# Kernel tuning notes

Measured on AMD Instinct MI355X. Metric: run time of the kernel, lower is better.

The kernel has to match this reference:

```python
import jax, jax.numpy as jnp
import numpy as np
from jax import lax

B, T, EPROJS, DUNITS, ATT_DIM = 32, 2048, 1024, 1024, 512
ACONV_CHANS, ACONV_FILTS = 10, 100
KSIZE = 2 * ACONV_FILTS + 1  # 201
SCALING = 2.0


def setup_inputs() -> dict:
    key = jax.random.key(0)
    ks = jax.random.split(key, 16)
    lengths = jax.random.randint(ks[1], (B,), T // 2, T + 1, dtype=jnp.int32)
    # normalized uniform initial attention over valid frames (as in module's init branch)
    mask = jnp.arange(T)[None, :] < lengths[:, None]
    att_prev = mask.astype(jnp.float32) / lengths[:, None].astype(jnp.float32)
    s_e = 1.0 / np.sqrt(EPROJS)
    s_d = 1.0 / np.sqrt(DUNITS)
    s_a = 1.0 / np.sqrt(ATT_DIM)
    s_c = 1.0 / np.sqrt(ACONV_CHANS)
    return {
        "enc_hs_pad": jax.random.normal(ks[0], (B, T, EPROJS), jnp.float32),
        "enc_hs_len": lengths,
        "dec_z": jax.random.normal(ks[2], (B, DUNITS), jnp.float32),
        "att_prev": att_prev,
        "att_h": jax.random.normal(ks[3], (B, ATT_DIM), jnp.float32) * 0.1,
        "att_c": jax.random.normal(ks[4], (B, ATT_DIM), jnp.float32) * 0.1,
        "W_enc": jax.random.uniform(ks[5], (EPROJS, ATT_DIM), jnp.float32, -s_e, s_e),
        "b_enc": jax.random.uniform(ks[6], (ATT_DIM,), jnp.float32, -s_e, s_e),
        "W_dec": jax.random.uniform(ks[7], (DUNITS, ATT_DIM), jnp.float32, -s_d, s_d),
        "W_conv": jax.random.uniform(ks[8], (ACONV_CHANS, 1, KSIZE), jnp.float32, -0.1, 0.1),
        "W_ih": jax.random.uniform(ks[9], (4 * ATT_DIM, ACONV_CHANS), jnp.float32, -s_a, s_a),
        "W_hh": jax.random.uniform(ks[10], (4 * ATT_DIM, ATT_DIM), jnp.float32, -s_a, s_a),
        "W_g": jax.random.uniform(ks[11], (ATT_DIM, 1), jnp.float32, -s_a, s_a),
        "b_g": jax.random.uniform(ks[12], (1,), jnp.float32, -s_a, s_a),
    }


def reference(enc_hs_pad, enc_hs_len, dec_z, att_prev, att_h, att_c,
              W_enc, b_enc, W_dec, W_conv, W_ih, W_hh, W_g, b_g):
    # pre_compute_enc_h = mlp_enc(enc_h): (B, T, A)
    pre_enc = jnp.einsum("bte,ea->bta", enc_hs_pad, W_enc) + b_enc

    # location conv over previous attention: (B,1,T) -> (B,C,T)
    conv = lax.conv_general_dilated(
        att_prev[:, None, :], W_conv,
        window_strides=(1,), padding=[(ACONV_FILTS, ACONV_FILTS)],
        dimension_numbers=("NCH", "OIH", "NCH"))
    # relu + global max-pool over T -> (B, C)
    conv_feat = jnp.max(jax.nn.relu(conv), axis=2)

    # LSTMCell (no bias), PyTorch gate order i, f, g, o
    gates = conv_feat @ W_ih.T + att_h @ W_hh.T  # (B, 4A)
    i, f, g, o = jnp.split(gates, 4, axis=1)
    c_new = jax.nn.sigmoid(f) * att_c + jax.nn.sigmoid(i) * jnp.tanh(g)
    h_new = jax.nn.sigmoid(o) * jnp.tanh(c_new)

    dec_t = dec_z @ W_dec  # (B, A)
    # scoring: gvec(tanh(att_h + pre_enc + dec)) -> (B, T)
    e = (jnp.tanh(h_new[:, None, :] + pre_enc + dec_t[:, None, :]) @ W_g)[..., 0] + b_g[0]

    pad_mask = jnp.arange(e.shape[1])[None, :] >= enc_hs_len[:, None]
    e = jnp.where(pad_mask, -jnp.inf, e)
    w = jax.nn.softmax(SCALING * e, axis=1)  # (B, T)

    c = jnp.einsum("bt,bte->be", w, enc_hs_pad)  # (B, EPROJS)
    return c, w, h_new, c_new
```

## Files before the change

### kernel.cpp

```cpp
#include <hip/hip_runtime.h>
#include <hip/hip_bf16.h>
#include <cstddef>

#define BB      32
#define TT_ALL  2048
#define EPROJS  1024
#define DUNITS  1024
#define ATT     512
#define CH      10
#define KS      201
#define FILT    100

#define OFF_C   0
#define OFF_W   (BB*EPROJS)
#define OFF_H   (OFF_W + BB*TT_ALL)
#define OFF_CN  (OFF_H + BB*ATT)

#define WS_CF    0
#define WS_V     512
#define WS_EP    16896
#define WS_WF    147968
#define WS_WT    213504
#define WS_PART  475648
#define WS_GP    737792
#define WS_DP    868864

typedef __attribute__((ext_vector_type(8))) short short8;
typedef __attribute__((ext_vector_type(4))) float f32x4;

__device__ __forceinline__ float sigm(float x) { return 1.f / (1.f + expf(-x)); }
__device__ __forceinline__ unsigned short f2bf(float f) {
  unsigned u = __float_as_uint(f);
  return (unsigned short)((u + 0x7FFFu + ((u >> 16) & 1u)) >> 16);
}
__device__ __forceinline__ ushort2 f2bf2(float a, float b) {
  __hip_bfloat162 h = __float22bfloat162_rn(float2{a, b});
  return *reinterpret_cast<ushort2*>(&h);
}
__device__ __forceinline__ short8 pack_bf16x8(const float4 a, const float4 b) {
  union { short8 s; ushort2 u[4]; } r;
  r.u[0] = f2bf2(a.x, a.y); r.u[1] = f2bf2(a.z, a.w);
  r.u[2] = f2bf2(b.x, b.y); r.u[3] = f2bf2(b.z, b.w);
  return r.s;
}

__global__ __launch_bounds__(64) void k_wprepF(const float* __restrict__ W,
                                               unsigned short* __restrict__ WTF) {
  const int r16 = blockIdx.x >> 5, ks = blockIdx.x & 31;
  const int l = threadIdx.x;
  const int a = r16 * 16 + (l & 15);
  const int e0 = ks * 32 + (l >> 4) * 8;
  union { short8 s; unsigned short h[8]; } r;
#pragma unroll
  for (int j = 0; j < 8; ++j) r.h[j] = f2bf(W[(size_t)(e0 + j) * ATT + a]);
  *reinterpret_cast<short8*>(&WTF[((size_t)(r16 * 32 + ks) * 64 + l) * 8]) = r.s;
}

__global__ __launch_bounds__(256) void k_conv(const float* __restrict__ att_prev,
                                              const float* __restrict__ W_conv,
                                              float* __restrict__ conv_feat) {
  const int b  = blockIdx.x / CH;
  const int ch = blockIdx.x % CH;
  __shared__ float sprev[TT_ALL + 2 * FILT];
  __shared__ float sw[KS];
  __shared__ float red[4];
  const int tid = threadIdx.x;
  for (int i = tid; i < TT_ALL + 2 * FILT; i += 256) {
    int t = i - FILT;
    sprev[i] = (t >= 0 && t < TT_ALL) ? att_prev[b * TT_ALL + t] : 0.f;
  }
  for (int i = tid; i < KS; i += 256) sw[i] = W_conv[ch * KS + i];
  __syncthreads();
  float m = 0.f;
  for (int t = tid; t < TT_ALL; t += 256) {
    float s = 0.f;
    for (int k = 0; k < KS; ++k) s = fmaf(sprev[t + k], sw[k], s);
    m = fmaxf(m, s);
  }
  for (int off = 32; off; off >>= 1) m = fmaxf(m, __shfl_xor(m, off, 64));
  if ((tid & 63) == 0) red[tid >> 6] = m;
  __syncthreads();
  if (tid == 0)
    conv_feat[b * CH + ch] = fmaxf(fmaxf(red[0], red[1]), fmaxf(red[2], red[3]));
}

__global__ __launch_bounds__(256) void k_gates(const float* __restrict__ att_h,
                                               const float* __restrict__ W_hh,
                                               float* __restrict__ gp) {
  const int jt = blockIdx.x >> 1;
  const int sp = blockIdx.x & 1;
  const int j0 = jt * 64;
  const int k0 = sp * 256;
  const int tid = threadIdx.x;
  const int al = tid & 63, bg = tid >> 6;
  __shared__ float sW[64][65];
  __shared__ float sH[32][64];
  float acc[8];
#pragma unroll
  for (int i = 0; i < 8; ++i) acc[i] = 0.f;
  for (int kc = 0; kc < 256; kc += 64) {
    __syncthreads();
#pragma unroll
    for (int i = 0; i < 4; ++i) {
      const int f = tid + i * 256;
      const int r = f >> 4, q = f & 15;
      const float4 w4 = *reinterpret_cast<const float4*>(
          &W_hh[(size_t)(j0 + r) * ATT + k0 + kc + q * 4]);
      sW[r][q * 4 + 0] = w4.x; sW[r][q * 4 + 1] = w4.y;
      sW[r][q * 4 + 2] = w4.z; sW[r][q * 4 + 3] = w4.w;
    }
#pragma unroll
    for (int i = 0; i < 2; ++i) {
      const int g = tid + i * 256;
      const int r = g >> 4, q = g & 15;
      *reinterpret_cast<float4*>(&sH[r][q * 4]) = *reinterpret_cast<const float4*>(
          &att_h[(size_t)r * ATT + k0 + kc + q * 4]);
    }
    __syncthreads();
#pragma unroll 16
    for (int k = 0; k < 64; ++k) {
      const float w = sW[al][k];
#pragma unroll
      for (int bb = 0; bb < 8; ++bb)
        acc[bb] = fmaf(w, sH[bg * 8 + bb][k], acc[bb]);
    }
  }
#pragma unroll
  for (int bb = 0; bb < 8; ++bb)
    gp[((size_t)(sp * 32 + bg * 8 + bb)) * (4 * ATT) + j0 + al] = acc[bb];
}

__global__ __launch_bounds__(256) void k_dec(const float* __restrict__ dec_z,
                                             const float* __restrict__ W_dec,
                                             float* __restrict__ dp) {
  const int at = blockIdx.x >> 1;
  const int sp = blockIdx.x & 1;
  const int a0 = at * 64;
  const int d0 = sp * 512;
  const int tid = threadIdx.x;
  const int al = tid & 63, bg = tid >> 6;
  __shared__ float sW[64][64];
  __shared__ float sZ[32][64];
  float acc[8];
#pragma unroll
  for (int i = 0; i < 8; ++i) acc[i] = 0.f;
  for (int dc = 0; dc < 512; dc += 64) {
    __syncthreads();
#pragma unroll
    for (int i = 0; i < 4; ++i) {
      const int f = tid + i * 256;
      const int r = f >> 4, q = f & 15;
      *reinterpret_cast<float4*>(&sW[r][q * 4]) = *reinterpret_cast<const float4*>(
          &W_dec[(size_t)(d0 + dc + r) * ATT + a0 + q * 4]);
    }
#pragma unroll
    for (int i = 0; i < 2; ++i) {
      const int g = tid + i * 256;
      const int r = g >> 4, q = g & 15;
      *reinterpret_cast<float4*>(&sZ[r][q * 4]) = *reinterpret_cast<const float4*>(
          &dec_z[(size_t)r * DUNITS + d0 + dc + q * 4]);
    }
    __syncthreads();
#pragma unroll 16
    for (int d = 0; d < 64; ++d) {
      const float w = sW[d][al];
#pragma unroll
      for (int bb = 0; bb < 8; ++bb)
        acc[bb] = fmaf(sZ[bg * 8 + bb][d], w, acc[bb]);
    }
  }
#pragma unroll
  for (int bb = 0; bb < 8; ++bb)
    dp[((size_t)(sp * 32 + bg * 8 + bb)) * ATT + a0 + al] = acc[bb];
}

__global__ __launch_bounds__(256) void k_lstm_v(const float* __restrict__ gp,
                                                const float* __restrict__ dp,
                                                const float* __restrict__ conv_feat,
                                                const float* __restrict__ W_ih,
                                                const float* __restrict__ att_c,
                                                float* __restrict__ v,
                                                float* __restrict__ out) {
  const int b = blockIdx.x, tid = threadIdx.x;
  __shared__ float scf[CH];
  if (tid < CH) scf[tid] = conv_feat[b * CH + tid];
  __syncthreads();
  for (int a = tid; a < ATT; a += 256) {
    float g4[4];
#pragma unroll
    for (int q = 0; q < 4; ++q) {
      const int j = q * ATT + a;
      float g = gp[(size_t)b * (4 * ATT) + j] + gp[(size_t)(32 + b) * (4 * ATT) + j];
#pragma unroll
      for (int c = 0; c < CH; ++c) g = fmaf(scf[c], W_ih[(size_t)j * CH + c], g);
      g4[q] = g;
    }
    const float ig = sigm(g4[0]);
    const float fg = sigm(g4[1]);
    const float gg = tanhf(g4[2]);
    const float og = sigm(g4[3]);
    const float cN = fg * att_c[b * ATT + a] + ig * gg;
    const float hN = og * tanhf(cN);
    out[OFF_H + b * ATT + a]  = hN;
    out[OFF_CN + b * ATT + a] = cN;
    v[b * ATT + a] = hN + dp[(size_t)b * ATT + a] + dp[(size_t)(32 + b) * ATT + a];
  }
}

__global__ __launch_bounds__(256, 4) void k_score_mfma(const float* __restrict__ enc,
                                                       const unsigned short* __restrict__ WTF,
                                                       const float* __restrict__ b_enc,
                                                       const float* __restrict__ W_g,
                                                       const float* __restrict__ v,
                                                       const int* __restrict__ lens,
                                                       float* __restrict__ ep) {
  const int bid = blockIdx.x;
  const int na = bid & 1;
  const int tt = (bid >> 1) & 31;
  const int b  = bid >> 6;
  const int t0 = tt * 64;
  if (t0 >= lens[b]) return;
  const int tid = threadIdx.x;
  const int lane = tid & 63, wn = tid >> 6;
  const int l15 = lane & 15, l4 = lane >> 4;

  __shared__ unsigned short sA[2][64][40];
  __shared__ float red[64][4];

  const int rowS = tid >> 2, qS = tid & 3;
  const float* pAg = enc + ((size_t)b * TT_ALL + t0 + rowS) * EPROJS + qS * 8;
  const int r16b = na * 16 + wn * 4;
  const unsigned short* pBf = WTF + (size_t)r16b * 32 * 512 + (size_t)lane * 8;

  f32x4 acc[4][4];
#pragma unroll
  for (int m = 0; m < 4; ++m)
#pragma unroll
    for (int n = 0; n < 4; ++n) acc[m][n] = (f32x4){0.f, 0.f, 0.f, 0.f};

  float4 a0 = *reinterpret_cast<const float4*>(pAg);
  float4 a1 = *reinterpret_cast<const float4*>(pAg + 4);

  for (int ks = 0; ks < 32; ++ks) {
    const int buf = ks & 1;
    *reinterpret_cast<short8*>(&sA[buf][rowS][qS * 8]) = pack_bf16x8(a0, a1);
    __syncthreads();
    if (ks + 1 < 32) {
      a0 = *reinterpret_cast<const float4*>(pAg + (ks + 1) * 32);
      a1 = *reinterpret_cast<const float4*>(pAg + (ks + 1) * 32 + 4);
    }
    short8 bfr[4];
#pragma unroll
    for (int n = 0; n < 4; ++n)
      bfr[n] = *reinterpret_cast<const short8*>(pBf + (size_t)(n * 32 + ks) * 512);
    short8 af[4];
#pragma unroll
    for (int m = 0; m < 4; ++m)
      af[m] = *reinterpret_cast<const short8*>(&sA[buf][16 * m + l15][l4 * 8]);
#pragma unroll
    for (int n = 0; n < 4; ++n)
#pragma unroll
      for (int m = 0; m < 4; ++m)
        acc[m][n] = __builtin_amdgcn_mfma_f32_16x16x32_bf16(af[m], bfr[n], acc[m][n], 0, 0, 0);
  }

  float rp[4][4];
#pragma unroll
  for (int m = 0; m < 4; ++m)
#pragma unroll
    for (int j = 0; j < 4; ++j) rp[m][j] = 0.f;
#pragma unroll
  for (int n = 0; n < 4; ++n) {
    const int a = na * 256 + wn * 64 + 16 * n + l15;
    const float va = v[b * ATT + a] + b_enc[a];
    const float wg = W_g[a];
#pragma unroll
    for (int m = 0; m < 4; ++m)
#pragma unroll
      for (int j = 0; j < 4; ++j) {
        const float x = acc[m][n][j] + va;
        const float th = 1.f - 2.f / (__expf(2.f * x) + 1.f);
        rp[m][j] = fmaf(th, wg, rp[m][j]);
      }
  }
#pragma unroll
  for (int m = 0; m < 4; ++m)
#pragma unroll
    for (int j = 0; j < 4; ++j) {
      float s = rp[m][j];
      s += __shfl_xor(s, 1, 64);
      s += __shfl_xor(s, 2, 64);
      s += __shfl_xor(s, 4, 64);
      s += __shfl_xor(s, 8, 64);
      rp[m][j] = s;
    }
  __syncthreads();
  if (l15 == 0) {
#pragma unroll
    for (int m = 0; m < 4; ++m)
#pragma unroll
      for (int j = 0; j < 4; ++j)
        red[16 * m + l4 * 4 + j][wn] = rp[m][j];
  }
  __syncthreads();
  if (tid < 64) {
    const float s = red[tid][0] + red[tid][1] + red[tid][2] + red[tid][3];
    ep[(size_t)na * (BB * TT_ALL) + b * TT_ALL + t0 + tid] = s;
  }
}

__global__ __launch_bounds__(256) void k_softmax(const float* __restrict__ ep,
                                                 const int* __restrict__ lens,
                                                 float* __restrict__ wf,
                                                 float* __restrict__ out) {
  const int b = blockIdx.x, tid = threadIdx.x, len = lens[b];
  __shared__ float sbuf[4];
  float vals[8];
  float m = -1e30f;
#pragma unroll
  for (int i = 0; i < 8; ++i) {
    const int t = tid + i * 256;
    const float x = (t < len)
        ? ep[b * TT_ALL + t] + ep[(size_t)BB * TT_ALL + b * TT_ALL + t] : -1e30f;
    vals[i] = x;
    m = fmaxf(m, x);
  }
  for (int off = 32; off; off >>= 1) m = fmaxf(m, __shfl_xor(m, off, 64));
  if ((tid & 63) == 0) sbuf[tid >> 6] = m;
  __syncthreads();
  m = fmaxf(fmaxf(sbuf[0], sbuf[1]), fmaxf(sbuf[2], sbuf[3]));
  __syncthreads();
  float s = 0.f;
#pragma unroll
  for (int i = 0; i < 8; ++i) {
    const int t = tid + i * 256;
    const float p = (t < len) ? expf(2.f * (vals[i] - m)) : 0.f;
    vals[i] = p;
    s += p;
  }
  for (int off = 32; off; off >>= 1) s += __shfl_xor(s, off, 64);
  if ((tid & 63) == 0) sbuf[tid >> 6] = s;
  __syncthreads();
  s = sbuf[0] + sbuf[1] + sbuf[2] + sbuf[3];
  const float inv = 1.f / s;
#pragma unroll
  for (int i = 0; i < 8; ++i) {
    const int t = tid + i * 256;
    const float wv = vals[i] * inv;
    wf[b * TT_ALL + t] = wv;
    out[OFF_W + b * TT_ALL + t] = wv;
  }
}

__global__ __launch_bounds__(256) void k_ctx(const float* __restrict__ enc,
                                             const float* __restrict__ wf,
                                             const int* __restrict__ lens,
                                             float* __restrict__ part) {
  const int blk = blockIdx.x;
  const int b  = blk >> 5;
  const int et = (blk >> 3) & 3;
  const int tc = blk & 7;
  const int tid = threadIdx.x;
  const int e = et * 256 + tid;
  const int len = lens[b];
  const int tbeg = tc * 256;
  const int tend = min(tbeg + 256, len);
  float a0 = 0.f, a1 = 0.f;
  int t = tbeg;
  for (; t + 2 <= tend; t += 2) {
    a0 = fmaf(wf[b * TT_ALL + t + 0], enc[((size_t)b * TT_ALL + t + 0) * EPROJS + e], a0);
    a1 = fmaf(wf[b * TT_ALL + t + 1], enc[((size_t)b * TT_ALL + t + 1) * EPROJS + e], a1);
  }
  for (; t < tend; ++t)
    a0 = fmaf(wf[b * TT_ALL + t], enc[((size_t)b * TT_ALL + t) * EPROJS + e], a0);
  part[((size_t)b * 8 + tc) * EPROJS + e] = a0 + a1;
}

__global__ __launch_bounds__(256) void k_comb(const float* __restrict__ part,
                                              float* __restrict__ out) {
  const int b = blockIdx.x >> 2, et = blockIdx.x & 3;
  const int e = et * 256 + threadIdx.x;
  float s = 0.f;
#pragma unroll
  for (int tc = 0; tc < 8; ++tc) s += part[((size_t)b * 8 + tc) * EPROJS + e];
  out[OFF_C + b * EPROJS + e] = s;
}

extern "C" void kernel_launch(void* const* d_in, const int* in_sizes, int n_in,
                              void* d_out, int out_size, void* d_ws, size_t ws_size,
                              hipStream_t stream) {
  const float* enc      = (const float*)d_in[0];
  const int*   lens     = (const int*)d_in[1];
  const float* dec_z    = (const float*)d_in[2];
  const float* att_prev = (const float*)d_in[3];
  const float* att_h    = (const float*)d_in[4];
  const float* att_c    = (const float*)d_in[5];
  const float* W_enc    = (const float*)d_in[6];
  const float* b_enc    = (const float*)d_in[7];
  const float* W_dec    = (const float*)d_in[8];
  const float* W_conv   = (const float*)d_in[9];
  const float* W_ih     = (const float*)d_in[10];
  const float* W_hh     = (const float*)d_in[11];
  const float* W_g      = (const float*)d_in[12];
  const float* b_g      = (const float*)d_in[13];
  (void)b_g;
  float* out = (float*)d_out;
  float* ws  = (float*)d_ws;

  float* cf   = ws + WS_CF;
  float* v    = ws + WS_V;
  float* ep   = ws + WS_EP;
  float* wf   = ws + WS_WF;
  unsigned short* wtf = (unsigned short*)(ws + WS_WT);
  float* part = ws + WS_PART;
  float* gp   = ws + WS_GP;
  float* dp   = ws + WS_DP;

  k_wprepF    <<<32 * 32, 64, 0, stream>>>(W_enc, wtf);
  k_conv      <<<BB * CH, 256, 0, stream>>>(att_prev, W_conv, cf);
  k_gates     <<<64, 256, 0, stream>>>(att_h, W_hh, gp);
  k_dec       <<<16, 256, 0, stream>>>(dec_z, W_dec, dp);
  k_lstm_v    <<<BB, 256, 0, stream>>>(gp, dp, cf, W_ih, att_c, v, out);
  k_score_mfma<<<BB * 32 * 2, 256, 0, stream>>>(enc, wtf, b_enc, W_g, v, lens, ep);
  k_softmax   <<<BB, 256, 0, stream>>>(ep, lens, wf, out);
  k_ctx       <<<BB * 32, 256, 0, stream>>>(enc, wf, lens, part);
  k_comb      <<<BB * 4, 256, 0, stream>>>(part, out);
}
```

Before: 236.4 us.

## Merge two ATT-half score blocks into one 512-thread block covering all ATT

The scoring GEMM block now covers all 512 attention columns with 8 waves instead of splitting them across two 256-thread blocks. Each encoder tile is therefore loaded from global memory and converted to bf16 once rather than twice. Each block writes a single score row directly, so the softmax no longer sums two partial buffers. In exchange, blocks are larger with fewer per CU and there are half as many blocks, which could reduce latency hiding.

```diff
diff --git a/kernel.cpp b/kernel.cpp
--- a/kernel.cpp
+++ b/kernel.cpp
@@ -18,12 +18,12 @@
 
 #define WS_CF    0
 #define WS_V     512
-#define WS_EP    16896
-#define WS_WF    147968
-#define WS_WT    213504
-#define WS_PART  475648
-#define WS_GP    737792
-#define WS_DP    868864
+#define WS_E     16896
+#define WS_WF    82432
+#define WS_WT    147968
+#define WS_PART  410112
+#define WS_GP    672256
+#define WS_DP    803328
 
 typedef __attribute__((ext_vector_type(8))) short short8;
 typedef __attribute__((ext_vector_type(4))) float f32x4;
@@ -36,12 +36,6 @@
 __device__ __forceinline__ ushort2 f2bf2(float a, float b) {
   __hip_bfloat162 h = __float22bfloat162_rn(float2{a, b});
   return *reinterpret_cast<ushort2*>(&h);
-}
-__device__ __forceinline__ short8 pack_bf16x8(const float4 a, const float4 b) {
-  union { short8 s; ushort2 u[4]; } r;
-  r.u[0] = f2bf2(a.x, a.y); r.u[1] = f2bf2(a.z, a.w);
-  r.u[2] = f2bf2(b.x, b.y); r.u[3] = f2bf2(b.z, b.w);
-  return r.s;
 }
 
 __global__ __launch_bounds__(64) void k_wprepF(const float* __restrict__ W,
@@ -207,17 +201,15 @@
   }
 }
 
-__global__ __launch_bounds__(256, 4) void k_score_mfma(const float* __restrict__ enc,
+__global__ __launch_bounds__(512, 2) void k_score_mfma(const float* __restrict__ enc,
                                                        const unsigned short* __restrict__ WTF,
                                                        const float* __restrict__ b_enc,
                                                        const float* __restrict__ W_g,
                                                        const float* __restrict__ v,
                                                        const int* __restrict__ lens,
-                                                       float* __restrict__ ep) {
-  const int bid = blockIdx.x;
-  const int na = bid & 1;
-  const int tt = (bid >> 1) & 31;
-  const int b  = bid >> 6;
+                                                       float* __restrict__ e_out) {
+  const int b  = blockIdx.x >> 5;
+  const int tt = blockIdx.x & 31;
   const int t0 = tt * 64;
   if (t0 >= lens[b]) return;
   const int tid = threadIdx.x;
@@ -225,12 +217,11 @@
   const int l15 = lane & 15, l4 = lane >> 4;
 
   __shared__ unsigned short sA[2][64][40];
-  __shared__ float red[64][4];
-
-  const int rowS = tid >> 2, qS = tid & 3;
-  const float* pAg = enc + ((size_t)b * TT_ALL + t0 + rowS) * EPROJS + qS * 8;
-  const int r16b = na * 16 + wn * 4;
-  const unsigned short* pBf = WTF + (size_t)r16b * 32 * 512 + (size_t)lane * 8;
+  __shared__ float red[64][8];
+
+  const int rowS = tid >> 3, qS = tid & 7;
+  const float* pAg = enc + ((size_t)b * TT_ALL + t0 + rowS) * EPROJS + qS * 4;
+  const unsigned short* pBf = WTF + (size_t)(wn * 4) * 32 * 512 + (size_t)lane * 8;
 
   f32x4 acc[4][4];
 #pragma unroll
@@ -239,16 +230,17 @@
     for (int n = 0; n < 4; ++n) acc[m][n] = (f32x4){0.f, 0.f, 0.f, 0.f};
 
   float4 a0 = *reinterpret_cast<const float4*>(pAg);
-  float4 a1 = *reinterpret_cast<const float4*>(pAg + 4);
 
   for (int ks = 0; ks < 32; ++ks) {
     const int buf = ks & 1;
-    *reinterpret_cast<short8*>(&sA[buf][rowS][qS * 8]) = pack_bf16x8(a0, a1);
+    {
+      const ushort2 h0 = f2bf2(a0.x, a0.y), h1 = f2bf2(a0.z, a0.w);
+      ushort4 h; h.x = h0.x; h.y = h0.y; h.z = h1.x; h.w = h1.y;
+      *reinterpret_cast<ushort4*>(&sA[buf][rowS][qS * 4]) = h;
+    }
     __syncthreads();
-    if (ks + 1 < 32) {
+    if (ks + 1 < 32)
       a0 = *reinterpret_cast<const float4*>(pAg + (ks + 1) * 32);
-      a1 = *reinterpret_cast<const float4*>(pAg + (ks + 1) * 32 + 4);
-    }
     short8 bfr[4];
 #pragma unroll
     for (int n = 0; n < 4; ++n)
@@ -271,7 +263,7 @@
     for (int j = 0; j < 4; ++j) rp[m][j] = 0.f;
 #pragma unroll
   for (int n = 0; n < 4; ++n) {
-    const int a = na * 256 + wn * 64 + 16 * n + l15;
+    const int a = wn * 64 + 16 * n + l15;
     const float va = v[b * ATT + a] + b_enc[a];
     const float wg = W_g[a];
 #pragma unroll
@@ -304,12 +296,14 @@
   }
   __syncthreads();
   if (tid < 64) {
-    const float s = red[tid][0] + red[tid][1] + red[tid][2] + red[tid][3];
-    ep[(size_t)na * (BB * TT_ALL) + b * TT_ALL + t0 + tid] = s;
-  }
-}
-
-__global__ __launch_bounds__(256) void k_softmax(const float* __restrict__ ep,
+    float s = 0.f;
+#pragma unroll
+    for (int q = 0; q < 8; ++q) s += red[tid][q];
+    e_out[b * TT_ALL + t0 + tid] = s;
+  }
+}
+
+__global__ __launch_bounds__(256) void k_softmax(const float* __restrict__ e,
                                                  const int* __restrict__ lens,
                                                  float* __restrict__ wf,
                                                  float* __restrict__ out) {
@@ -320,8 +314,7 @@
 #pragma unroll
   for (int i = 0; i < 8; ++i) {
     const int t = tid + i * 256;
-    const float x = (t < len)
-        ? ep[b * TT_ALL + t] + ep[(size_t)BB * TT_ALL + b * TT_ALL + t] : -1e30f;
+    const float x = (t < len) ? e[b * TT_ALL + t] : -1e30f;
     vals[i] = x;
     m = fmaxf(m, x);
   }
@@ -409,7 +402,7 @@
 
   float* cf   = ws + WS_CF;
   float* v    = ws + WS_V;
-  float* ep   = ws + WS_EP;
+  float* e_s  = ws + WS_E;
   float* wf   = ws + WS_WF;
   unsigned short* wtf = (unsigned short*)(ws + WS_WT);
   float* part = ws + WS_PART;
@@ -421,8 +414,8 @@
   k_gates     <<<64, 256, 0, stream>>>(att_h, W_hh, gp);
   k_dec       <<<16, 256, 0, stream>>>(dec_z, W_dec, dp);
   k_lstm_v    <<<BB, 256, 0, stream>>>(gp, dp, cf, W_ih, att_c, v, out);
-  k_score_mfma<<<BB * 32 * 2, 256, 0, stream>>>(enc, wtf, b_enc, W_g, v, lens, ep);
-  k_softmax   <<<BB, 256, 0, stream>>>(ep, lens, wf, out);
+  k_score_mfma<<<BB * 32, 512, 0, stream>>>(enc, wtf, b_enc, W_g, v, lens, e_s);
+  k_softmax   <<<BB, 256, 0, stream>>>(e_s, lens, wf, out);
   k_ctx       <<<BB * 32, 256, 0, stream>>>(enc, wf, lens, part);
   k_comb      <<<BB * 4, 256, 0, stream>>>(part, out);
 }
```

New measurement: 226.1 us. 4.4% less time.
